# Kernel optimization log

Measured on AMD Instinct MI355X. Metric: run time of the kernel, lower is better.

Reference implementation:

```python
import jax, jax.numpy as jnp
import numpy as np

C = 768
H = 12
HD = C // H  # 64


def setup_inputs() -> dict:
    key = jax.random.key(0)
    k1, k2, k3, k4, k5, k6 = jax.random.split(key, 6)
    B, T = 8, 1024
    x = jax.random.normal(k1, (B, T, C), dtype=jnp.float32)
    mask = jax.random.randint(k2, (B, T), 0, 2, dtype=jnp.int32)
    # Linear params stored so that y = x @ W + b (W is [in, out])
    W_attn = jax.random.normal(k3, (C, 3 * C), dtype=jnp.float32) * 0.02
    b_attn = jax.random.normal(k4, (3 * C,), dtype=jnp.float32) * 0.02
    W_proj = jax.random.normal(k5, (C, C), dtype=jnp.float32) * 0.02
    b_proj = jax.random.normal(k6, (C,), dtype=jnp.float32) * 0.02
    return {"x": x, "mask": mask, "W_attn": W_attn, "b_attn": b_attn,
            "W_proj": W_proj, "b_proj": b_proj}


def reference(x, mask, W_attn, b_attn, W_proj, b_proj):
    B, T, _ = x.shape
    qkv = x @ W_attn + b_attn                      # [B, T, 3C]
    q, k, v = jnp.split(qkv, 3, axis=2)            # each [B, T, C]
    # [B, T, C] -> [B, H, T, HD]
    q = q.reshape(B, T, H, HD).transpose(0, 2, 1, 3)
    k = k.reshape(B, T, H, HD).transpose(0, 2, 1, 3)
    v = v.reshape(B, T, H, HD).transpose(0, 2, 1, 3)

    scale = 1.0 / np.sqrt(HD).astype(np.float32)
    att = jnp.einsum('bhqd,bhkd->bhqk', q, k) * scale  # [B, H, T, T]

    causal = jnp.tril(jnp.ones((T, T), dtype=bool))    # [T, T]
    att = jnp.where(causal[None, None], att, -jnp.inf)

    # custom mask: per-(batch, query-row) flag; where mask==0 the whole row
    # of scores is overwritten with 0.0001 (AFTER causal fill, as in torch)
    row_masked = (mask == 0)[:, None, :, None]         # [B, 1, T, 1]
    att = jnp.where(row_masked, jnp.float32(1e-4), att)

    att = jax.nn.softmax(att, axis=-1)
    # dropout layers are identity in eval mode
    y = jnp.einsum('bhqk,bhkd->bhqd', att, v)          # [B, H, T, HD]
    y = y.transpose(0, 2, 1, 3).reshape(B, T, C)
    y = y @ W_proj + b_proj
    return y
```

## Files before the change

kernel.cpp:

```cpp
#include <hip/hip_runtime.h>

#define BQ 8
#define TT 1024
#define CC 768
#define NH 12
#define HD 64
#define BH (BQ*NH)
#define MROWS (BQ*TT)
#define NQKV (3*CC)
#define KD CC

typedef unsigned short u16;
typedef __attribute__((ext_vector_type(4))) short short4v;
typedef __attribute__((ext_vector_type(8))) short short8v;
typedef __attribute__((ext_vector_type(4))) float floatx4;
typedef __attribute__((address_space(1))) const unsigned int gu32;
typedef __attribute__((address_space(3))) unsigned int lu32;

__device__ __forceinline__ float bf2f(u16 u) {
  union { unsigned int i; float f; } c; c.i = ((unsigned int)u) << 16; return c.f;
}
__device__ __forceinline__ u16 f2bf(float f) {
  union { float f; unsigned int i; } c; c.f = f;
  unsigned int i = c.i;
  return (u16)((i + 0x7FFFu + ((i >> 16) & 1u)) >> 16);
}
__device__ __forceinline__ float fast_exp2(float x) {
  return __builtin_amdgcn_exp2f(x);
}
__device__ __forceinline__ void async_ld16(const u16* g, u16* l) {
  __builtin_amdgcn_global_load_lds((gu32*)g, (lu32*)l, 16, 0, 0);
}

#define PREP_CONV 6144
#define PREP_WA   1728
#define PREP_WP   576
#define PREP_TOTAL (PREP_CONV + PREP_WA + PREP_WP)

__global__ __launch_bounds__(256) void prep_kernel(
    const float* __restrict__ x, u16* __restrict__ xb,
    const float* __restrict__ Wattn, u16* __restrict__ WtA,
    const float* __restrict__ Wproj, u16* __restrict__ WtP)
{
  __shared__ float tile[32][33];
  int bid = blockIdx.x;
  int tid = threadIdx.x;
  if (bid < PREP_CONV) {
    int i = (bid * 256 + tid) * 4;
    floatx4 v = *(const floatx4*)(x + i);
    short4v o;
    o[0] = (short)f2bf(v[0]); o[1] = (short)f2bf(v[1]);
    o[2] = (short)f2bf(v[2]); o[3] = (short)f2bf(v[3]);
    *(short4v*)(xb + i) = o;
    return;
  }
  const float* in; u16* out; int R, Cc, b2;
  if (bid < PREP_CONV + PREP_WA) { in = Wattn; out = WtA; R = KD; Cc = NQKV; b2 = bid - PREP_CONV; }
  else                           { in = Wproj; out = WtP; R = CC; Cc = CC;   b2 = bid - PREP_CONV - PREP_WA; }
  int ct = Cc >> 5;
  int bx = b2 % ct;
  int by = b2 / ct;
  int tx = tid & 31;
  int ty = tid >> 5;
  int c0 = bx << 5, r0 = by << 5;
#pragma unroll
  for (int s = 0; s < 4; ++s)
    tile[ty + s*8][tx] = in[(size_t)(r0 + ty + s*8) * Cc + c0 + tx];
  __syncthreads();
#pragma unroll
  for (int s = 0; s < 4; ++s)
    out[(size_t)(c0 + ty + s*8) * R + r0 + tx] = f2bf(tile[tx][ty + s*8]);
}

__global__ __launch_bounds__(256) void gemm_bt(
    const u16* __restrict__ A, const u16* __restrict__ Bt,
    const float* __restrict__ bias,
    float* __restrict__ out,
    u16* __restrict__ qo, u16* __restrict__ ko, u16* __restrict__ vo,
    int M, int N, int mode)
{
  __shared__ u16 smem[64 * 64 + 128 * 64];
  u16* Asm = smem;
  u16* Bsm = smem + 64 * 64;

  int tid = threadIdx.x;
  int lane = tid & 63;
  int w = tid >> 6;
  int c = lane & 15;
  int q4 = lane >> 4;

  int mtiles = M >> 6;
  int mt = blockIdx.x % mtiles;
  int nt = blockIdx.x / mtiles;
  int m0 = mt << 6, n0 = nt << 7;

  int wr = (w >> 1) << 5;
  int wc = (w & 1) << 6;

  int srow8 = lane >> 3;
  int ug = ((lane & 7) ^ srow8) << 3;
  const u16* ag = A  + (size_t)(m0 + w * 16 + srow8) * KD + ug;
  const u16* bg = Bt + (size_t)(n0 + w * 32 + srow8) * KD + ug;
  u16* asl = &Asm[(w * 16) * 64];
  u16* bsl = &Bsm[(w * 32) * 64];

  floatx4 acc[2][4];
#pragma unroll
  for (int mi = 0; mi < 2; ++mi)
#pragma unroll
    for (int ni = 0; ni < 4; ++ni) acc[mi][ni] = (floatx4){0.f, 0.f, 0.f, 0.f};

  int c7 = c & 7;

#pragma unroll 1
  for (int kt = 0; kt < KD; kt += 64) {
    async_ld16(ag + kt,              asl);
    async_ld16(ag + kt + 8 * KD,     asl + 8 * 64);
    async_ld16(bg + kt,              bsl);
    async_ld16(bg + kt + 8 * KD,     bsl + 8 * 64);
    async_ld16(bg + kt + 16 * KD,    bsl + 16 * 64);
    async_ld16(bg + kt + 24 * KD,    bsl + 24 * 64);
    __syncthreads();

    short8v af[2][2], bf[4][2];
#pragma unroll
    for (int kc = 0; kc < 2; ++kc) {
      int uoff = ((kc * 4 + q4) ^ c7) << 3;
#pragma unroll
      for (int mi = 0; mi < 2; ++mi)
        af[mi][kc] = *(const short8v*)&Asm[(wr + mi * 16 + c) * 64 + uoff];
#pragma unroll
      for (int ni = 0; ni < 4; ++ni)
        bf[ni][kc] = *(const short8v*)&Bsm[(wc + ni * 16 + c) * 64 + uoff];
    }
#pragma unroll
    for (int kc = 0; kc < 2; ++kc)
#pragma unroll
      for (int mi = 0; mi < 2; ++mi)
#pragma unroll
        for (int ni = 0; ni < 4; ++ni)
          acc[mi][ni] = __builtin_amdgcn_mfma_f32_16x16x32_bf16(af[mi][kc], bf[ni][kc], acc[mi][ni], 0, 0, 0);
    __syncthreads();
  }

  if (mode == 0) {
    int which = (n0 + wc) / CC;
    int nbase = (n0 + wc) - which * CC;
    int bb = m0 >> 10;
    int t0 = m0 & 1023;

    if (which < 2) {
      u16* dst0 = (which == 0) ? qo : ko;
#pragma unroll
      for (int ni = 0; ni < 4; ++ni) {
        int nn = nbase + ni * 16 + c;
        int hh = nn >> 6, dd = nn & 63;
        float bv = bias[which * CC + nn];
#pragma unroll
        for (int mi = 0; mi < 2; ++mi) {
#pragma unroll
          for (int r = 0; r < 4; ++r) {
            int tt2 = t0 + wr + mi * 16 + q4 * 4 + r;
            dst0[(((size_t)(bb * NH + hh)) * TT + tt2) * HD + dd] = f2bf(acc[mi][ni][r] + bv);
          }
        }
      }
    }
    if (n0 + 127 >= 2 * CC) {
      u16* Ct = smem;
      if (which == 2) {
#pragma unroll
        for (int ni = 0; ni < 4; ++ni) {
          float bv = bias[2 * CC + nbase + ni * 16 + c];
#pragma unroll
          for (int mi = 0; mi < 2; ++mi) {
            short4v pk;
#pragma unroll
            for (int r = 0; r < 4; ++r) pk[r] = (short)f2bf(acc[mi][ni][r] + bv);
            *(short4v*)&Ct[(wc + ni * 16 + c) * 72 + wr + mi * 16 + q4 * 4] = pk;
          }
        }
      }
      __syncthreads();
#pragma unroll
      for (int j = 0; j < 4; ++j) {
        int flat = tid + j * 256;
        int drow = flat >> 3, u = flat & 7;
        int nn2 = n0 + drow;
        if (nn2 >= 2 * CC) {
          int nv = nn2 - 2 * CC;
          int h2 = nv >> 6, d2 = nv & 63;
          short8v val = *(const short8v*)&Ct[drow * 72 + u * 8];
          *(short8v*)&vo[(((size_t)(bb * NH + h2)) * HD + d2) * TT + t0 + u * 8] = val;
        }
      }
    }
  } else {
#pragma unroll
    for (int ni = 0; ni < 4; ++ni) {
      int nn = n0 + wc + ni * 16 + c;
      float bv = bias[nn];
#pragma unroll
      for (int mi = 0; mi < 2; ++mi) {
#pragma unroll
        for (int r = 0; r < 4; ++r) {
          int mm = m0 + wr + mi * 16 + q4 * 4 + r;
          out[(size_t)mm * N + nn] = acc[mi][ni][r] + bv;
        }
      }
    }
  }
}

__global__ __launch_bounds__(256) void gemm_proj(
    const u16* __restrict__ A, const u16* __restrict__ Bt,
    const float* __restrict__ bias, float* __restrict__ out)
{
  __shared__ u16 As[64 * 64];
  __shared__ u16 Bs[64 * 64];

  int tid = threadIdx.x;
  int lane = tid & 63;
  int w = tid >> 6;
  int c = lane & 15;
  int q4 = lane >> 4;

  int mt = blockIdx.x & 127;
  int nt = blockIdx.x >> 7;
  int m0 = mt << 6, n0 = nt << 6;

  int wr = (w >> 1) << 5;
  int wc = (w & 1) << 5;

  int srow8 = lane >> 3;
  int ug = ((lane & 7) ^ srow8) << 3;
  const u16* ag = A  + (size_t)(m0 + w * 16 + srow8) * KD + ug;
  const u16* bg = Bt + (size_t)(n0 + w * 16 + srow8) * KD + ug;
  u16* asl = &As[(w * 16) * 64];
  u16* bsl = &Bs[(w * 16) * 64];

  floatx4 acc[2][2];
#pragma unroll
  for (int mi = 0; mi < 2; ++mi)
#pragma unroll
    for (int ni = 0; ni < 2; ++ni) acc[mi][ni] = (floatx4){0.f, 0.f, 0.f, 0.f};

  int c7 = c & 7;

#pragma unroll 1
  for (int kt = 0; kt < KD; kt += 64) {
    async_ld16(ag + kt,          asl);
    async_ld16(ag + kt + 8 * KD, asl + 8 * 64);
    async_ld16(bg + kt,          bsl);
    async_ld16(bg + kt + 8 * KD, bsl + 8 * 64);
    __syncthreads();

    short8v af[2][2], bf[2][2];
#pragma unroll
    for (int kc = 0; kc < 2; ++kc) {
      int uoff = ((kc * 4 + q4) ^ c7) << 3;
#pragma unroll
      for (int mi = 0; mi < 2; ++mi)
        af[mi][kc] = *(const short8v*)&As[(wr + mi * 16 + c) * 64 + uoff];
#pragma unroll
      for (int ni = 0; ni < 2; ++ni)
        bf[ni][kc] = *(const short8v*)&Bs[(wc + ni * 16 + c) * 64 + uoff];
    }
#pragma unroll
    for (int kc = 0; kc < 2; ++kc)
#pragma unroll
      for (int mi = 0; mi < 2; ++mi)
#pragma unroll
        for (int ni = 0; ni < 2; ++ni)
          acc[mi][ni] = __builtin_amdgcn_mfma_f32_16x16x32_bf16(af[mi][kc], bf[ni][kc], acc[mi][ni], 0, 0, 0);
    __syncthreads();
  }

#pragma unroll
  for (int ni = 0; ni < 2; ++ni) {
    int nn = n0 + wc + ni * 16 + c;
    float bv = bias[nn];
#pragma unroll
    for (int mi = 0; mi < 2; ++mi) {
#pragma unroll
      for (int r = 0; r < 4; ++r) {
        int mm = m0 + wr + mi * 16 + q4 * 4 + r;
        out[(size_t)mm * CC + nn] = acc[mi][ni][r] + bv;
      }
    }
  }
}

__global__ __launch_bounds__(256) void vmean_kernel(
    const u16* __restrict__ vtb, float* __restrict__ mv)
{
  int bh = blockIdx.x;
  int tid = threadIdx.x;
  int d = tid >> 2;
  int q = tid & 3;
  const u16* p = vtb + ((size_t)bh * HD + d) * TT + q * 256;
  float s = 0.f;
#pragma unroll 4
  for (int j = 0; j < 256; j += 8) {
    short8v v = *(const short8v*)(p + j);
#pragma unroll
    for (int i = 0; i < 8; ++i) s += bf2f((u16)v[i]);
  }
  s += __shfl_xor(s, 1);
  s += __shfl_xor(s, 2);
  if (q == 0) mv[bh * HD + d] = s * (1.0f / 1024.0f);
}

#define LDW 72
#define SCL 0.18033688f

__global__ __launch_bounds__(256) void attn_kernel(
    const u16* __restrict__ qb, const u16* __restrict__ kb,
    const u16* __restrict__ vtb, const int* __restrict__ mask,
    const float* __restrict__ meanv,
    u16* __restrict__ outb)
{
  __shared__ u16 Ks[2][64 * LDW];
  __shared__ u16 Vs[2][64 * LDW];
  __shared__ u16 Ps[4][16 * LDW];

  int tid = threadIdx.x;
  int lane = tid & 63;
  int w = tid >> 6;
  int c = lane & 15;
  int q4 = lane >> 4;

  int pair = blockIdx.x & 7;
  int bh = blockIdx.x >> 3;
  int b = bh / NH;
  int h = bh - b * NH;

  int srow = tid >> 2;
  int schunk = (tid & 3) << 4;
  const u16* kgp = kb + ((size_t)bh * TT + srow) * HD + schunk;
  const u16* vgp = vtb + ((size_t)bh * HD + srow) * TT + schunk;
  u16* pw = &Ps[w][0];

  short8v onesv;
#pragma unroll
  for (int j = 0; j < 8; ++j) onesv[j] = (short)0x3F80;

#pragma unroll 1
  for (int phase = 0; phase < 2; ++phase) {
    int qt = phase ? (15 - pair) : pair;
    int rowbase = (qt << 6) + (w << 4);

    short8v qfrag[2];
    {
      const u16* qp = qb + ((size_t)bh * TT + rowbase + c) * HD + q4 * 8;
      qfrag[0] = *(const short8v*)qp;
      qfrag[1] = *(const short8v*)(qp + 32);
    }

    floatx4 o[4];
#pragma unroll
    for (int i = 0; i < 4; ++i) o[i] = (floatx4){0.f, 0.f, 0.f, 0.f};
    floatx4 o5 = (floatx4){0.f, 0.f, 0.f, 0.f};

    short8v kr0 = *(const short8v*)kgp;
    short8v kr1 = *(const short8v*)(kgp + 8);
    short8v vr0 = *(const short8v*)vgp;
    short8v vr1 = *(const short8v*)(vgp + 8);
    __syncthreads();
    {
      u16* kd = &Ks[0][srow * LDW + schunk];
      u16* vd = &Vs[0][srow * LDW + schunk];
      *(short8v*)kd = kr0; *(short8v*)(kd + 8) = kr1;
      *(short8v*)vd = vr0; *(short8v*)(vd + 8) = vr1;
    }

#pragma unroll 1
    for (int kt = 0; kt <= qt; ++kt) {
      int cur = kt & 1;
      __syncthreads();

      if (kt < qt) {
        const u16* kp = kgp + ((size_t)(kt + 1) << 6) * HD;
        const u16* vp = vgp + ((kt + 1) << 6);
        kr0 = *(const short8v*)kp;
        kr1 = *(const short8v*)(kp + 8);
        vr0 = *(const short8v*)vp;
        vr1 = *(const short8v*)(vp + 8);
      }

      floatx4 s[4];
#pragma unroll
      for (int nt = 0; nt < 4; ++nt) s[nt] = (floatx4){0.f, 0.f, 0.f, 0.f};
      __builtin_amdgcn_s_setprio(1);
#pragma unroll
      for (int kc = 0; kc < 2; ++kc) {
#pragma unroll
        for (int nt = 0; nt < 4; ++nt) {
          short8v kf = *(const short8v*)&Ks[cur][(nt * 16 + c) * LDW + kc * 32 + q4 * 8];
          s[nt] = __builtin_amdgcn_mfma_f32_16x16x32_bf16(kf, qfrag[kc], s[nt], 0, 0, 0);
        }
      }
      __builtin_amdgcn_s_setprio(0);

      int qrl = (w << 4) + c;
#pragma unroll
      for (int nt = 0; nt < 4; ++nt) {
        short4v pk;
#pragma unroll
        for (int r = 0; r < 4; ++r) {
          float sv = s[nt][r];
          if (kt == qt && (nt * 16 + (q4 << 2) + r > qrl)) sv = -INFINITY;
          pk[r] = (short)f2bf(fast_exp2(sv * SCL));
        }
        *(short4v*)&pw[c * LDW + nt * 16 + (q4 << 2)] = pk;
      }

      if (kt < qt) {
        u16* kd = &Ks[cur ^ 1][srow * LDW + schunk];
        u16* vd = &Vs[cur ^ 1][srow * LDW + schunk];
        *(short8v*)kd = kr0; *(short8v*)(kd + 8) = kr1;
        *(short8v*)vd = vr0; *(short8v*)(vd + 8) = vr1;
      }

      __builtin_amdgcn_s_setprio(1);
#pragma unroll
      for (int kc = 0; kc < 2; ++kc) {
        short8v pf = *(const short8v*)&pw[c * LDW + kc * 32 + q4 * 8];
#pragma unroll
        for (int nt = 0; nt < 4; ++nt) {
          short8v vf = *(const short8v*)&Vs[cur][(nt * 16 + c) * LDW + kc * 32 + q4 * 8];
          o[nt] = __builtin_amdgcn_mfma_f32_16x16x32_bf16(pf, vf, o[nt], 0, 0, 0);
        }
        o5 = __builtin_amdgcn_mfma_f32_16x16x32_bf16(pf, onesv, o5, 0, 0, 0);
      }
      __builtin_amdgcn_s_setprio(0);
    }

    int qrow[4]; bool msk[4]; float inv[4];
#pragma unroll
    for (int r = 0; r < 4; ++r) {
      qrow[r] = rowbase + q4 * 4 + r;
      msk[r] = (mask[b * TT + qrow[r]] == 0);
      inv[r] = 1.f / o5[r];
    }
#pragma unroll
    for (int nt = 0; nt < 4; ++nt) {
      int d = nt * 16 + c;
      float mv = meanv[bh * HD + d];
#pragma unroll
      for (int r = 0; r < 4; ++r) {
        float val = msk[r] ? mv : o[nt][r] * inv[r];
        outb[((size_t)(b * TT + qrow[r])) * CC + h * HD + d] = f2bf(val);
      }
    }
  }
}

extern "C" void kernel_launch(void* const* d_in, const int* in_sizes, int n_in,
                              void* d_out, int out_size, void* d_ws, size_t ws_size,
                              hipStream_t stream)
{
  (void)in_sizes; (void)n_in; (void)out_size; (void)ws_size;
  const float* x     = (const float*)d_in[0];
  const int*   mask  = (const int*)d_in[1];
  const float* Wattn = (const float*)d_in[2];
  const float* battn = (const float*)d_in[3];
  const float* Wproj = (const float*)d_in[4];
  const float* bproj = (const float*)d_in[5];
  float* out = (float*)d_out;

  char* ws = (char*)d_ws;
  size_t off = 0;
  auto alloc = [&](size_t bytes) -> void* {
    void* p = ws + off;
    off += (bytes + 255) & ~(size_t)255;
    return p;
  };
  u16* WtA  = (u16*)alloc((size_t)NQKV * KD * 2);
  u16* WtP  = (u16*)alloc((size_t)CC * CC * 2);
  u16* xb   = (u16*)alloc((size_t)MROWS * CC * 2);
  u16* qbuf = (u16*)alloc((size_t)MROWS * CC * 2);
  u16* kbuf = (u16*)alloc((size_t)MROWS * CC * 2);
  u16* vtb  = (u16*)alloc((size_t)MROWS * CC * 2);
  u16* abuf = (u16*)alloc((size_t)MROWS * CC * 2);
  float* mv = (float*)alloc((size_t)BH * HD * 4);

  prep_kernel<<<PREP_TOTAL, 256, 0, stream>>>(x, xb, Wattn, WtA, Wproj, WtP);

  gemm_bt<<<(MROWS/64)*(NQKV/128), 256, 0, stream>>>(
      xb, WtA, battn, nullptr, qbuf, kbuf, vtb, MROWS, NQKV, 0);

  vmean_kernel<<<BH, 256, 0, stream>>>(vtb, mv);

  attn_kernel<<<BH * 8, 256, 0, stream>>>(qbuf, kbuf, vtb, mask, mv, abuf);

  gemm_proj<<<(MROWS/64)*(CC/64), 256, 0, stream>>>(abuf, WtP, bproj, out);
}
```

Baseline: 189.6 us.

## Fuse V-mean reduction into QKV GEMM epilogue and remap attention block order

Removes the separate vmean kernel. Per-column V sums are accumulated with shuffles and atomicAdd inside the QKV GEMM epilogue, on a buffer zeroed by an extra prep block, and the attention kernel scales by 1/1024. The attention block index is also permuted so consecutive blocks cover different heads, which changes scheduling and load balance. Costs added: atomics in the GEMM epilogue and a mean taken from fp32 accumulators rather than the bf16-rounded V, so float summation order is no longer deterministic.

```diff
diff --git a/kernel.cpp b/kernel.cpp
--- a/kernel.cpp
+++ b/kernel.cpp
@@ -40,11 +40,16 @@
 __global__ __launch_bounds__(256) void prep_kernel(
     const float* __restrict__ x, u16* __restrict__ xb,
     const float* __restrict__ Wattn, u16* __restrict__ WtA,
-    const float* __restrict__ Wproj, u16* __restrict__ WtP)
+    const float* __restrict__ Wproj, u16* __restrict__ WtP,
+    float* __restrict__ mvz)
 {
   __shared__ float tile[32][33];
   int bid = blockIdx.x;
   int tid = threadIdx.x;
+  if (bid == PREP_TOTAL) {
+    for (int i = tid; i < BH * HD; i += 256) mvz[i] = 0.f;
+    return;
+  }
   if (bid < PREP_CONV) {
     int i = (bid * 256 + tid) * 4;
     floatx4 v = *(const floatx4*)(x + i);
@@ -77,6 +82,7 @@
     const float* __restrict__ bias,
     float* __restrict__ out,
     u16* __restrict__ qo, u16* __restrict__ ko, u16* __restrict__ vo,
+    float* __restrict__ mvp,
     int M, int N, int mode)
 {
   __shared__ u16 smem[64 * 64 + 128 * 64];
@@ -194,6 +200,22 @@
           *(short8v*)&vo[(((size_t)(bb * NH + h2)) * HD + d2) * TT + t0 + u * 8] = val;
         }
       }
+      if (which == 2) {
+        int hw = nbase >> 6;
+        int bhw = bb * NH + hw;
+#pragma unroll
+        for (int ni = 0; ni < 4; ++ni) {
+          float bv = bias[2 * CC + nbase + ni * 16 + c];
+          float s = 8.0f * bv;
+#pragma unroll
+          for (int mi = 0; mi < 2; ++mi)
+#pragma unroll
+            for (int r = 0; r < 4; ++r) s += acc[mi][ni][r];
+          s += __shfl_xor(s, 16);
+          s += __shfl_xor(s, 32);
+          if (q4 == 0) atomicAdd(&mvp[bhw * HD + ni * 16 + c], s);
+        }
+      }
     }
   } else {
 #pragma unroll
@@ -289,26 +311,6 @@
       }
     }
   }
-}
-
-__global__ __launch_bounds__(256) void vmean_kernel(
-    const u16* __restrict__ vtb, float* __restrict__ mv)
-{
-  int bh = blockIdx.x;
-  int tid = threadIdx.x;
-  int d = tid >> 2;
-  int q = tid & 3;
-  const u16* p = vtb + ((size_t)bh * HD + d) * TT + q * 256;
-  float s = 0.f;
-#pragma unroll 4
-  for (int j = 0; j < 256; j += 8) {
-    short8v v = *(const short8v*)(p + j);
-#pragma unroll
-    for (int i = 0; i < 8; ++i) s += bf2f((u16)v[i]);
-  }
-  s += __shfl_xor(s, 1);
-  s += __shfl_xor(s, 2);
-  if (q == 0) mv[bh * HD + d] = s * (1.0f / 1024.0f);
 }
 
 #define LDW 72
@@ -330,8 +332,9 @@
   int c = lane & 15;
   int q4 = lane >> 4;
 
-  int pair = blockIdx.x & 7;
-  int bh = blockIdx.x >> 3;
+  int lbid = ((blockIdx.x & 7) * 96) + (blockIdx.x >> 3);
+  int pair = lbid & 7;
+  int bh = lbid >> 3;
   int b = bh / NH;
   int h = bh - b * NH;
 
@@ -446,7 +449,7 @@
 #pragma unroll
     for (int nt = 0; nt < 4; ++nt) {
       int d = nt * 16 + c;
-      float mv = meanv[bh * HD + d];
+      float mv = meanv[bh * HD + d] * 0.0009765625f;
 #pragma unroll
       for (int r = 0; r < 4; ++r) {
         float val = msk[r] ? mv : o[nt][r] * inv[r];
@@ -485,12 +488,10 @@
   u16* abuf = (u16*)alloc((size_t)MROWS * CC * 2);
   float* mv = (float*)alloc((size_t)BH * HD * 4);
 
-  prep_kernel<<<PREP_TOTAL, 256, 0, stream>>>(x, xb, Wattn, WtA, Wproj, WtP);
+  prep_kernel<<<PREP_TOTAL + 1, 256, 0, stream>>>(x, xb, Wattn, WtA, Wproj, WtP, mv);
 
   gemm_bt<<<(MROWS/64)*(NQKV/128), 256, 0, stream>>>(
-      xb, WtA, battn, nullptr, qbuf, kbuf, vtb, MROWS, NQKV, 0);
-
-  vmean_kernel<<<BH, 256, 0, stream>>>(vtb, mv);
+      xb, WtA, battn, nullptr, qbuf, kbuf, vtb, mv, MROWS, NQKV, 0);
 
   attn_kernel<<<BH * 8, 256, 0, stream>>>(qbuf, kbuf, vtb, mask, mv, abuf);
 
```

New measurement: 180.6 us. -4.7%, faster.
